# Optimization experiments

Measured on AMD Instinct MI355X. Metric: run time of the kernel, lower is better.

The kernel has to match this reference:

```python
import jax, jax.numpy as jnp
import numpy as np

B, S, D, H, HD, I = 8, 512, 2048, 32, 64, 8192
REL = 2 * 512 - 1  # 1023
EPS = 1e-6
SCALE = float(np.sqrt(HD))


def _layernorm(x, g, b):
    mu = jnp.mean(x, axis=-1, keepdims=True)
    var = jnp.mean(jnp.square(x - mu), axis=-1, keepdims=True)
    return (x - mu) / jnp.sqrt(var + EPS) * g + b


def setup_inputs() -> dict:
    key = jax.random.key(0)
    ks = jax.random.split(key, 10)
    s = 0.02
    return {
        "hidden_states": jax.random.normal(ks[0], (B, S, D), dtype=jnp.float32),
        "wq": jax.random.normal(ks[1], (D, D), dtype=jnp.float32) * s,
        "wk": jax.random.normal(ks[2], (D, D), dtype=jnp.float32) * s,
        "wv": jax.random.normal(ks[3], (D, D), dtype=jnp.float32) * s,
        "wo": jax.random.normal(ks[4], (D, D), dtype=jnp.float32) * s,
        "rel_pos": jax.random.normal(ks[5], (REL, HD), dtype=jnp.float32),
        "ln1_g": jnp.ones((D,), jnp.float32),
        "ln1_b": jnp.zeros((D,), jnp.float32),
        "gate_w": jax.random.normal(ks[6], (D, I), dtype=jnp.float32) * s,
        "up_w": jax.random.normal(ks[7], (D, I), dtype=jnp.float32) * s,
        "down_w": jax.random.normal(ks[8], (I, D), dtype=jnp.float32) * s,
        "ln2_g": jnp.ones((D,), jnp.float32),
        "ln2_b": jnp.zeros((D,), jnp.float32),
    }


def reference(hidden_states, wq, wk, wv, wo, rel_pos, ln1_g, ln1_b,
              gate_w, up_w, down_w, ln2_g, ln2_b):
    x = hidden_states
    # --- MultiHeadAttentionXL ---
    q = (x @ wq).reshape(B, S, H, HD)
    k = (x @ wk).reshape(B, S, H, HD)
    v = (x @ wv).reshape(B, S, H, HD)
    scores = jnp.einsum('bqhd,bkhd->bhqk', q, k) / SCALE
    # relative position bias (seq_len <= 512 path)
    pos = jnp.arange(S)
    rp = jnp.clip(pos[None, :] - pos[:, None] + 512 - 1, 0, REL - 1)  # [S,S]
    bias = rel_pos[rp].mean(axis=-1)  # [S,S]
    scores = scores + bias[None, None]
    attn = jax.nn.softmax(scores, axis=-1)
    ctx = jnp.einsum('bhqk,bkhd->bqhd', attn, v).reshape(B, S, D)
    attn_out = ctx @ wo
    # residual + post-LN
    h = _layernorm(x + attn_out, ln1_g, ln1_b)
    # --- FeedForwardXL (SwiGLU) ---
    gate = jax.nn.silu(h @ gate_w)
    up = h @ up_w
    ffn = (gate * up) @ down_w
    h = _layernorm(h + ffn, ln2_g, ln2_b)
    return h
```

## Files before the change

kernel.cpp:

```cpp
#include <hip/hip_runtime.h>
#include <cstdint>
#include <cstddef>

typedef _Float16 f16;
typedef _Float16 f16x8 __attribute__((ext_vector_type(8)));
typedef _Float16 f16x4 __attribute__((ext_vector_type(4)));
typedef float    f32x4 __attribute__((ext_vector_type(4)));

constexpr int S_ = 512, D_ = 2048, H_ = 32, HD_ = 64, I_ = 8192;
constexpr int M_ = 4096;
constexpr int IH_ = 4096;

enum { OP_F32 = 0, OP_QKT = 3, OP_PV = 4, OP_QKV = 6, OP_GU = 9, OP_ADD = 10 };

__device__ __forceinline__ void gl_lds16(const void* g, void* lds) {
  __builtin_amdgcn_global_load_lds(
      (const __attribute__((address_space(1))) void*)g,
      (__attribute__((address_space(3))) void*)lds, 16, 0, 0);
}

template <int BM, int BN, int WR, int WC, int OP, int BK>
__global__ __launch_bounds__(256, 2) void gemm_k(
    const f16* __restrict__ A, int lda,
    const f16* __restrict__ B, int ldb,
    void* __restrict__ Cp, int ldc,
    int K, int bh0, const float* __restrict__ relmean,
    const f16* __restrict__ B2) {
  static_assert(WR * WC == 4, "4-wave blocks assumed");
  static_assert(BK == 32 || BK == 64, "");
  constexpr bool GU = (OP == OP_GU);
  constexpr int WM = BM / WR, WN = BN / WC;
  constexpr int IM = WM / 16, IN = WN / 16;
  constexpr int RR = (BK == 64) ? 8 : 16;
  constexpr int CA = BM * BK / 2048;
  constexpr int CB = BN * BK / 2048;
  constexpr int KS = BK / 32;
  __shared__ __align__(16) f16 As[BM * BK];
  __shared__ __align__(16) f16 Bs[(GU ? 2 : 1) * BN * BK];
  const int tid = threadIdx.x, wave = tid >> 6, lane = tid & 63;
  const int wm = wave / WC, wn = wave % WC;
  const int bn = blockIdx.x, bm = blockIdx.y, bz = blockIdx.z;

  long aoff = 0, boff = 0;
  if constexpr (OP == OP_QKT) {
    int bh = bh0 + bz;
    long hb = (long)(bh >> 5) * (S_ * D_) + (long)(bh & (H_ - 1)) * HD_;
    aoff = hb; boff = hb;
  }
  if constexpr (OP == OP_PV) {
    int bh = bh0 + bz;
    aoff = (long)bz * S_ * S_;
    boff = (long)bh * HD_ * S_;
  }
  if constexpr (OP == OP_QKV) boff = (long)bz * D_ * D_;

  const f16* Ab = A + aoff + (long)bm * BM * lda;
  const f16* Bb = B + boff + (long)bn * BN * ldb;
  const f16* Bb2 = nullptr;
  if constexpr (GU) Bb2 = B2 + (long)bn * BN * ldb;

  f32x4 acc[IM][IN], acc2[GU ? IM : 1][GU ? IN : 1];
#pragma unroll
  for (int i = 0; i < IM; i++)
#pragma unroll
    for (int j = 0; j < IN; j++) {
      acc[i][j] = {0.f, 0.f, 0.f, 0.f};
      if constexpr (GU) acc2[i][j] = {0.f, 0.f, 0.f, 0.f};
    }

  const int lrr = (BK == 64) ? (lane >> 3) : (lane >> 2);
  const int lcc = (BK == 64) ? (lane & 7) : (lane & 3);
  const int scc = (BK == 64) ? (lcc ^ (lrr & 7)) : lcc;
  const int g = lane >> 4, l15 = lane & 15;

  for (int kt = 0; kt < K; kt += BK) {
    if (kt) __syncthreads();
#pragma unroll
    for (int c = 0; c < CA; c++) {
      int reg = wave * CA + c;
      gl_lds16(Ab + (long)(reg * RR + lrr) * lda + kt + scc * 8, &As[reg * 512]);
    }
#pragma unroll
    for (int c = 0; c < CB; c++) {
      int reg = wave * CB + c;
      gl_lds16(Bb + (long)(reg * RR + lrr) * ldb + kt + scc * 8, &Bs[reg * 512]);
      if constexpr (GU)
        gl_lds16(Bb2 + (long)(reg * RR + lrr) * ldb + kt + scc * 8,
                 &Bs[BN * BK + reg * 512]);
    }
    __syncthreads();
    f16x8 af[KS][IM], bf[KS][IN], bf2[GU ? KS : 1][GU ? IN : 1];
#pragma unroll
    for (int s = 0; s < KS; s++) {
#pragma unroll
      for (int i = 0; i < IM; i++) {
        int row = wm * WM + i * 16 + l15;
        int cidx = s * 4 + g;
        if constexpr (BK == 64) cidx ^= (row & 7);
        af[s][i] = *(const f16x8*)&As[row * BK + cidx * 8];
      }
#pragma unroll
      for (int j = 0; j < IN; j++) {
        int colL = wn * WN + j * 16 + l15;
        int cidx = s * 4 + g;
        if constexpr (BK == 64) cidx ^= (colL & 7);
        bf[s][j] = *(const f16x8*)&Bs[colL * BK + cidx * 8];
        if constexpr (GU) bf2[s][j] = *(const f16x8*)&Bs[BN * BK + colL * BK + cidx * 8];
      }
    }
#pragma unroll
    for (int s = 0; s < KS; s++)
#pragma unroll
      for (int i = 0; i < IM; i++)
#pragma unroll
        for (int j = 0; j < IN; j++) {
          acc[i][j] = __builtin_amdgcn_mfma_f32_16x16x32_f16(af[s][i], bf[s][j], acc[i][j], 0, 0, 0);
          if constexpr (GU)
            acc2[i][j] = __builtin_amdgcn_mfma_f32_16x16x32_f16(af[s][i], bf2[s][j], acc2[i][j], 0, 0, 0);
        }
  }

  const int r0 = bm * BM + wm * WM + (lane >> 4) * 4;
  const int c0 = bn * BN + wn * WN + l15;
#pragma unroll
  for (int i = 0; i < IM; i++) {
#pragma unroll
    for (int j = 0; j < IN; j++) {
      int rowb = r0 + i * 16;
      int col = c0 + j * 16;
      if constexpr (OP == OP_F32) {
        float* C = (float*)Cp;
#pragma unroll
        for (int t = 0; t < 4; t++) C[(long)(rowb + t) * ldc + col] = acc[i][j][t];
      } else if constexpr (OP == OP_ADD) {
        float* C = (float*)Cp;
#pragma unroll
        for (int t = 0; t < 4; t++) C[(long)(rowb + t) * ldc + col] += acc[i][j][t];
      } else if constexpr (OP == OP_GU) {
        f16* C = (f16*)Cp;
#pragma unroll
        for (int t = 0; t < 4; t++) {
          float gg = acc[i][j][t], u = acc2[i][j][t];
          C[(long)(rowb + t) * ldc + col] = (f16)(gg / (1.f + __expf(-gg)) * u);
        }
      } else if constexpr (OP == OP_QKT) {
        f16* C = (f16*)Cp + (long)bz * S_ * S_;
#pragma unroll
        for (int t = 0; t < 4; t++) {
          int r = rowb + t;
          C[(long)r * S_ + col] = (f16)(acc[i][j][t] * 0.125f + relmean[col - r + 511]);
        }
      } else if constexpr (OP == OP_PV) {
        int bh = bh0 + bz;
        f16* C = (f16*)Cp + (long)(bh >> 5) * (S_ * D_) + (long)(bh & (H_ - 1)) * HD_;
#pragma unroll
        for (int t = 0; t < 4; t++) C[(long)(rowb + t) * ldc + col] = (f16)acc[i][j][t];
      } else if constexpr (OP == OP_QKV) {
        f16* C = (f16*)Cp;
        if (bz < 2) {
          f16* Cq = C + (long)bz * M_ * D_;
#pragma unroll
          for (int t = 0; t < 4; t++) Cq[(long)(rowb + t) * ldc + col] = (f16)acc[i][j][t];
        } else {
          f16* Cv = C + (long)2 * M_ * D_;
          int b = rowb >> 9, s0 = rowb & 511, h = col >> 6, hd = col & 63;
          f16x4 pk;
#pragma unroll
          for (int t = 0; t < 4; t++) pk[t] = (f16)acc[i][j][t];
          *(f16x4*)&Cv[((long)(b * H_ + h) * HD_ + hd) * S_ + s0] = pk;
        }
      }
    }
  }
}

__global__ __launch_bounds__(512, 2) void fattn_k(
    const f16* __restrict__ Q, const f16* __restrict__ Kg,
    const f16* __restrict__ Vt, f16* __restrict__ Ctx,
    const float* __restrict__ rel) {
  __shared__ __align__(16) f16 Ks[512 * 64];
  __shared__ __align__(16) f16 Vs[64 * 512];
  __shared__ float rms[1024];
  const int tid = threadIdx.x, wave = tid >> 6, lane = tid & 63;
  const int g = lane >> 4, l15 = lane & 15;
  const int lrr = lane >> 3, lcc = lane & 7;
  const int bm = blockIdx.x, bh = blockIdx.y;
  const int b = bh >> 5, h = bh & 31;
  const long qrow0 = (long)b * S_ + bm * 128;
  const long krow0 = (long)b * S_;
  const int hoff = h * HD_;

#pragma unroll
  for (int c = 0; c < 8; c++) {
    int reg = wave * 8 + c;
    gl_lds16(Kg + (krow0 + reg * 8 + lrr) * D_ + hoff + (lcc ^ lrr) * 8,
             &Ks[reg * 512]);
  }
  const f16* vb = Vt + (long)bh * HD_ * S_;
#pragma unroll
  for (int c = 0; c < 8; c++) {
    int reg = wave * 8 + c;
    int rb = reg >> 3, cb = reg & 7;
    gl_lds16(vb + (long)(rb * 8 + lrr) * S_ + cb * 64 + (lcc ^ lrr) * 8,
             &Vs[reg * 512]);
  }
  for (int i = tid; i < 1023; i += 512) rms[i] = rel[i];

  f16x8 aq[2];
#pragma unroll
  for (int ks = 0; ks < 2; ks++)
    aq[ks] = *(const f16x8*)&Q[(qrow0 + wave * 16 + l15) * D_ + hoff + ks * 32 + g * 8];

  __syncthreads();

  f32x4 acc[32];
#pragma unroll
  for (int jn = 0; jn < 32; jn++) acc[jn] = {0.f, 0.f, 0.f, 0.f};
#pragma unroll
  for (int jn = 0; jn < 32; jn++) {
    int r = jn * 16 + l15;
    f16x8 b0 = *(const f16x8*)&Ks[r * 64 + ((g) ^ (r & 7)) * 8];
    f16x8 b1 = *(const f16x8*)&Ks[r * 64 + ((4 + g) ^ (r & 7)) * 8];
    acc[jn] = __builtin_amdgcn_mfma_f32_16x16x32_f16(aq[0], b0, acc[jn], 0, 0, 0);
    acc[jn] = __builtin_amdgcn_mfma_f32_16x16x32_f16(aq[1], b1, acc[jn], 0, 0, 0);
  }

  const int qr0 = bm * 128 + wave * 16 + g * 4;
  float mx[4] = {-1e30f, -1e30f, -1e30f, -1e30f}, sum[4] = {0.f, 0.f, 0.f, 0.f};
#pragma unroll
  for (int t = 0; t < 4; t++) {
    int bb = l15 - (qr0 + t) + 511;
#pragma unroll
    for (int jn = 0; jn < 32; jn++) {
      float v = acc[jn][t] * 0.125f + rms[bb + jn * 16];
      acc[jn][t] = v;
      mx[t] = fmaxf(mx[t], v);
    }
  }
#pragma unroll
  for (int off = 8; off; off >>= 1)
#pragma unroll
    for (int t = 0; t < 4; t++) mx[t] = fmaxf(mx[t], __shfl_xor(mx[t], off));
#pragma unroll
  for (int t = 0; t < 4; t++)
#pragma unroll
    for (int jn = 0; jn < 32; jn++) {
      float e = __expf(acc[jn][t] - mx[t]);
      acc[jn][t] = e;
      sum[t] += e;
    }
#pragma unroll
  for (int off = 8; off; off >>= 1)
#pragma unroll
    for (int t = 0; t < 4; t++) sum[t] += __shfl_xor(sum[t], off);
  float rs[4];
#pragma unroll
  for (int t = 0; t < 4; t++) rs[t] = 1.f / sum[t];

  __syncthreads();

  f16* Pb = &Ks[wave * 4096];
  f32x4 aco[4];
#pragma unroll
  for (int jv = 0; jv < 4; jv++) aco[jv] = {0.f, 0.f, 0.f, 0.f};
#pragma unroll
  for (int hh = 0; hh < 2; hh++) {
#pragma unroll
    for (int jl = 0; jl < 16; jl++) {
      int jn = hh * 16 + jl;
      f16x4 w;
#pragma unroll
      for (int t = 0; t < 4; t++) w[t] = (f16)(acc[jn][t] * rs[t]);
      *(f16x4*)&Pb[(jl * 16 + l15) * 16 + g * 4] = w;
    }
#pragma unroll
    for (int kl = 0; kl < 8; kl++) {
      f16x8 ap;
#pragma unroll
      for (int i = 0; i < 8; i++)
        ap[i] = Pb[(kl * 32 + g * 8 + i) * 16 + l15];
#pragma unroll
      for (int jv = 0; jv < 4; jv++) {
        int r = jv * 16 + l15, c = (hh * 8 + kl) * 4 + g;
        f16x8 bv = *(const f16x8*)&Vs[(r >> 3) * 4096 + (c >> 3) * 512 +
                                      (r & 7) * 64 + ((c & 7) ^ (r & 7)) * 8];
        aco[jv] = __builtin_amdgcn_mfma_f32_16x16x32_f16(ap, bv, aco[jv], 0, 0, 0);
      }
    }
  }

#pragma unroll
  for (int jv = 0; jv < 4; jv++)
#pragma unroll
    for (int t = 0; t < 4; t++)
      Ctx[(qrow0 + wave * 16 + g * 4 + t) * D_ + hoff + jv * 16 + l15] =
          (f16)aco[jv][t];
}

__global__ __launch_bounds__(256) void transpose_k(
    const float* __restrict__ in, int ldin, int k0, int n0,
    f16* __restrict__ out, int ldout) {
  __shared__ f16 t[64][68];
  const int kb = blockIdx.x * 64, nb = blockIdx.y * 64;
  const int tid = threadIdx.x;
  {
    const int kr = tid >> 4, nc = (tid & 15) * 4;
    const float* src = in + (long)(k0 + kb) * ldin + (n0 + nb);
#pragma unroll
    for (int i = 0; i < 4; i++) {
      int k = kr + i * 16;
      f32x4 v = *(const f32x4*)&src[(long)k * ldin + nc];
#pragma unroll
      for (int j = 0; j < 4; j++) t[nc + j][k] = (f16)v[j];
    }
  }
  __syncthreads();
  {
    const int n = tid >> 2, kc = (tid & 3) * 16;
    f16* dst = out + (long)(nb + n) * ldout + (kb + kc);
#pragma unroll
    for (int j = 0; j < 4; j++)
      *(f16x4*)&dst[j * 4] = *(const f16x4*)&t[n][kc + j * 4];
  }
}

__global__ void cvt_f16_k(const float* __restrict__ in, f16* __restrict__ out, int n4) {
  int i = blockIdx.x * 256 + threadIdx.x;
  if (i >= n4) return;
  f32x4 v = ((const f32x4*)in)[i];
  f16x4 o;
#pragma unroll
  for (int t = 0; t < 4; t++) o[t] = (f16)v[t];
  ((f16x4*)out)[i] = o;
}

__global__ void relmean_k(const float* __restrict__ rel, float* __restrict__ rm) {
  int i = blockIdx.x * 256 + threadIdx.x;
  if (i >= 1023) return;
  float s = 0.f;
#pragma unroll 8
  for (int d = 0; d < 64; d++) s += rel[i * 64 + d];
  rm[i] = s * (1.f / 64.f);
}

__global__ __launch_bounds__(256) void ln1_k(const float* __restrict__ X,
                                             const float* __restrict__ Y,
                                             const float* __restrict__ g,
                                             const float* __restrict__ b,
                                             f16* __restrict__ outH) {
  int row = blockIdx.x;
  const float* x = X + (long)row * D_;
  const float* y = Y + (long)row * D_;
  int t = threadIdx.x;
  float v[8], sum = 0.f, sq = 0.f;
#pragma unroll
  for (int i = 0; i < 8; i++) {
    int idx = t + i * 256;
    float val = x[idx] + y[idx];
    v[i] = val; sum += val; sq += val * val;
  }
  for (int off = 32; off; off >>= 1) { sum += __shfl_down(sum, off); sq += __shfl_down(sq, off); }
  __shared__ float s1[4], s2[4];
  if ((t & 63) == 0) { s1[t >> 6] = sum; s2[t >> 6] = sq; }
  __syncthreads();
  sum = s1[0] + s1[1] + s1[2] + s1[3];
  sq = s2[0] + s2[1] + s2[2] + s2[3];
  float mu = sum * (1.f / D_);
  float rstd = rsqrtf(sq * (1.f / D_) - mu * mu + 1e-6f);
#pragma unroll
  for (int i = 0; i < 8; i++) {
    int idx = t + i * 256;
    outH[(long)row * D_ + idx] = (f16)((v[i] - mu) * rstd * g[idx] + b[idx]);
  }
}

__global__ __launch_bounds__(256) void ln2f_k(const float* __restrict__ X,
                                              const f16* __restrict__ Y,
                                              const float* __restrict__ g,
                                              const float* __restrict__ b,
                                              float* __restrict__ outF) {
  int row = blockIdx.x;
  const float* x = X + (long)row * D_;
  const f16* y = Y + (long)row * D_;
  int t = threadIdx.x;
  float v[8], sum = 0.f, sq = 0.f;
#pragma unroll
  for (int i = 0; i < 8; i++) {
    int idx = t + i * 256;
    float val = x[idx] + (float)y[idx];
    v[i] = val; sum += val; sq += val * val;
  }
  for (int off = 32; off; off >>= 1) { sum += __shfl_down(sum, off); sq += __shfl_down(sq, off); }
  __shared__ float s1[4], s2[4];
  if ((t & 63) == 0) { s1[t >> 6] = sum; s2[t >> 6] = sq; }
  __syncthreads();
  sum = s1[0] + s1[1] + s1[2] + s1[3];
  sq = s2[0] + s2[1] + s2[2] + s2[3];
  float mu = sum * (1.f / D_);
  float rstd = rsqrtf(sq * (1.f / D_) - mu * mu + 1e-6f);
#pragma unroll
  for (int i = 0; i < 8; i++) {
    int idx = t + i * 256;
    outF[(long)row * D_ + idx] = (v[i] - mu) * rstd * g[idx] + b[idx];
  }
}

extern "C" void kernel_launch(void* const* d_in, const int* in_sizes, int n_in,
                              void* d_out, int out_size, void* d_ws, size_t ws_size,
                              hipStream_t stream) {
  const float* x    = (const float*)d_in[0];
  const float* wq   = (const float*)d_in[1];
  const float* wk   = (const float*)d_in[2];
  const float* wv   = (const float*)d_in[3];
  const float* wo   = (const float*)d_in[4];
  const float* rel  = (const float*)d_in[5];
  const float* ln1g = (const float*)d_in[6];
  const float* ln1b = (const float*)d_in[7];
  const float* gw   = (const float*)d_in[8];
  const float* uw   = (const float*)d_in[9];
  const float* dw   = (const float*)d_in[10];
  const float* ln2g = (const float*)d_in[11];
  const float* ln2b = (const float*)d_in[12];
  float* out = (float*)d_out;

  constexpr size_t MD2 = (size_t)M_ * D_ * 2;
  if (ws_size < 8 * MD2 + 4096) return;
  char* w = (char*)d_ws;
  f16* qb   = (f16*)(w + 0 * MD2);
  f16* vT   = (f16*)(w + 2 * MD2);
  f16* xb   = (f16*)(w + 3 * MD2);
  f16* s45  = (f16*)(w + 4 * MD2);
  f16* h1h  = (f16*)(w + 6 * MD2);
  f16* s7   = (f16*)(w + 7 * MD2);
  float* relmean = (float*)(w + 8 * MD2);
  f16* ctxb = xb;
  float* attn_out = (float*)qb;
  f16* wqT  = s45;
  f16* woT  = s7;
  f16* gwTh = qb;
  f16* uwTh = (f16*)(w + 1 * MD2);
  f16* gch  = vT;
  f16* dwTh = s7;
  float* facc = (float*)s45;

  cvt_f16_k<<<M_ * D_ / 4 / 256, 256, 0, stream>>>(x, xb, M_ * D_ / 4);
  relmean_k<<<4, 256, 0, stream>>>(rel, relmean);
  transpose_k<<<dim3(32, 32), 256, 0, stream>>>(wq, D_, 0, 0, wqT, D_);
  transpose_k<<<dim3(32, 32), 256, 0, stream>>>(wk, D_, 0, 0, wqT + (size_t)D_ * D_, D_);
  transpose_k<<<dim3(32, 32), 256, 0, stream>>>(wv, D_, 0, 0, wqT + 2 * (size_t)D_ * D_, D_);
  transpose_k<<<dim3(32, 32), 256, 0, stream>>>(wo, D_, 0, 0, woT, D_);

  gemm_k<128, 128, 2, 2, OP_QKV, 32><<<dim3(16, 32, 3), 256, 0, stream>>>(
      xb, D_, wqT, D_, qb, D_, D_, 0, nullptr, nullptr);

  fattn_k<<<dim3(4, 256), 512, 0, stream>>>(
      qb, qb + (size_t)M_ * D_, vT, ctxb, relmean);

  gemm_k<128, 128, 2, 2, OP_F32, 32><<<dim3(16, 32, 1), 256, 0, stream>>>(
      ctxb, D_, woT, D_, attn_out, D_, D_, 0, nullptr, nullptr);
  ln1_k<<<M_, 256, 0, stream>>>(x, attn_out, ln1g, ln1b, h1h);

  for (int h = 0; h < 2; h++) {
    transpose_k<<<dim3(32, 64), 256, 0, stream>>>(gw, I_, 0, h * IH_, gwTh, D_);
    transpose_k<<<dim3(32, 64), 256, 0, stream>>>(uw, I_, 0, h * IH_, uwTh, D_);
    transpose_k<<<dim3(64, 32), 256, 0, stream>>>(dw, D_, h * IH_, 0, dwTh, IH_);
    gemm_k<128, 128, 2, 2, OP_GU, 32><<<dim3(IH_ / 128, 32, 1), 256, 0, stream>>>(
        h1h, D_, gwTh, D_, gch, IH_, D_, 0, nullptr, uwTh);
    if (h == 0)
      gemm_k<128, 128, 2, 2, OP_F32, 32><<<dim3(16, 32, 1), 256, 0, stream>>>(
          gch, IH_, dwTh, IH_, facc, D_, IH_, 0, nullptr, nullptr);
    else
      gemm_k<128, 128, 2, 2, OP_ADD, 32><<<dim3(16, 32, 1), 256, 0, stream>>>(
          gch, IH_, dwTh, IH_, facc, D_, IH_, 0, nullptr, nullptr);
  }
  ln2f_k<<<M_, 256, 0, stream>>>(facc, h1h, ln2g, ln2b, out);
}
```

Measured before the change: 1.086 ms.

## Add 256x256 8-wave pipelined GEMM for QKV and split gate/up projections

Introduces a new 512-thread GEMM kernel with 256x256 tiles, 64-wide K steps, swizzled LDS, direct global-to-LDS loads and a four-phase interleaved load/MFMA schedule with priority hints. It replaces the 128x128 GEMM for the fused QKV projection. The combined gate/up kernel is split into a SiLU pass followed by an up pass that multiplies the stored gate in place. Larger tiles are meant to cut global/LDS traffic per FLOP and hide load latency, at the cost of an extra read/write of the gate buffer and more register pressure.

```diff
diff --git a/kernel.cpp b/kernel.cpp
--- a/kernel.cpp
+++ b/kernel.cpp
@@ -11,12 +11,178 @@
 constexpr int M_ = 4096;
 constexpr int IH_ = 4096;
 
-enum { OP_F32 = 0, OP_QKT = 3, OP_PV = 4, OP_QKV = 6, OP_GU = 9, OP_ADD = 10 };
+enum { OP_F32 = 0, OP_QKT = 3, OP_PV = 4, OP_QKV = 6, OP_GU = 9, OP_ADD = 10,
+       OP_SILU = 11, OP_UPG = 12 };
 
 __device__ __forceinline__ void gl_lds16(const void* g, void* lds) {
   __builtin_amdgcn_global_load_lds(
       (const __attribute__((address_space(1))) void*)g,
       (__attribute__((address_space(3))) void*)lds, 16, 0, 0);
+}
+
+template <int MH, int NH>
+__device__ __forceinline__ void mfma_q(f32x4 (&acc)[8][4],
+                                       const f16x8 (&ra)[2][4],
+                                       const f16x8 (&rb)[2][2]) {
+#pragma unroll
+  for (int ks = 0; ks < 2; ks++)
+#pragma unroll
+    for (int i = 0; i < 4; i++)
+#pragma unroll
+      for (int j = 0; j < 2; j++)
+        acc[MH * 4 + i][NH * 2 + j] = __builtin_amdgcn_mfma_f32_16x16x32_f16(
+            ra[ks][i], rb[ks][j], acc[MH * 4 + i][NH * 2 + j], 0, 0, 0);
+}
+
+template <int OP>
+__global__ __launch_bounds__(512, 2) void gemm8_k(
+    const f16* __restrict__ A, int lda,
+    const f16* __restrict__ B, int ldb,
+    void* __restrict__ Cp, int ldc, int K,
+    const f16* __restrict__ G) {
+  __shared__ __align__(16) f16 As[2 * 2 * 128 * 64];
+  __shared__ __align__(16) f16 Bs[2 * 2 * 128 * 64];
+  const int tid = threadIdx.x, wave = tid >> 6, lane = tid & 63;
+  const int wm = wave >> 2, wn = wave & 3;
+  const int g = lane >> 4, l15 = lane & 15;
+  const int lr8 = lane >> 3, lc8 = lane & 7;
+  const int bn = blockIdx.x, bm = blockIdx.y;
+  const f16* Ab = A + (long)bm * 256 * lda;
+  const f16* Bb = B + (long)bn * 256 * ldb;
+  const int sc_src = lc8 ^ (((lr8 >> 2) & 1) << 1);
+  const int swz_rd = ((l15 >> 2) & 1) << 1;
+
+  f32x4 acc[8][4];
+#pragma unroll
+  for (int i = 0; i < 8; i++)
+#pragma unroll
+    for (int j = 0; j < 4; j++) acc[i][j] = {0.f, 0.f, 0.f, 0.f};
+
+  int aoff[2][4], boff[2][2];
+#pragma unroll
+  for (int ks = 0; ks < 2; ks++) {
+#pragma unroll
+    for (int i = 0; i < 4; i++)
+      aoff[ks][i] = (i * 16 + l15) * 64 + ((ks * 4 + g) ^ swz_rd) * 8;
+#pragma unroll
+    for (int j = 0; j < 2; j++)
+      boff[ks][j] = ((wn & 1) * 64 + j * 16 + l15) * 64 + ((ks * 4 + g) ^ swz_rd) * 8;
+  }
+
+  auto stA = [&](int buf, int half, int kt) {
+#pragma unroll
+    for (int c = 0; c < 2; c++)
+      gl_lds16(Ab + (long)(half * 128 + (wave * 2 + c) * 8 + lr8) * lda + kt + sc_src * 8,
+               &As[buf * 16384 + half * 8192 + (wave * 2 + c) * 512]);
+  };
+  auto stB = [&](int buf, int half, int kt) {
+#pragma unroll
+    for (int c = 0; c < 2; c++)
+      gl_lds16(Bb + (long)(half * 128 + (wave * 2 + c) * 8 + lr8) * ldb + kt + sc_src * 8,
+               &Bs[buf * 16384 + half * 8192 + (wave * 2 + c) * 512]);
+  };
+
+  const int NT = K / 64;
+  stB(0, 0, 0); stB(0, 1, 0); stA(0, 0, 0); stA(0, 1, 0);
+  stB(1, 0, 64); stB(1, 1, 64);
+  asm volatile("s_waitcnt vmcnt(4)" ::: "memory");
+  __builtin_amdgcn_s_barrier();
+
+  f16x8 ra[2][4], rb0[2][2], rb1[2][2];
+  for (int T = 0; T < NT; T++) {
+    const int buf = T & 1, kt = T * 64;
+    const f16* Ah = &As[buf * 16384 + wm * 8192];
+    const f16* Bh = &Bs[buf * 16384 + (wn >> 1) * 8192];
+#pragma unroll
+    for (int ks = 0; ks < 2; ks++) {
+#pragma unroll
+      for (int i = 0; i < 4; i++) ra[ks][i] = *(const f16x8*)&Ah[aoff[ks][i]];
+#pragma unroll
+      for (int j = 0; j < 2; j++) rb0[ks][j] = *(const f16x8*)&Bh[boff[ks][j]];
+    }
+    if (T + 1 < NT) stA(buf ^ 1, 0, kt + 64);
+    __builtin_amdgcn_s_barrier();
+    asm volatile("s_waitcnt lgkmcnt(0)" ::: "memory");
+    __builtin_amdgcn_sched_barrier(0);
+    __builtin_amdgcn_s_setprio(1);
+    mfma_q<0, 0>(acc, ra, rb0);
+    __builtin_amdgcn_s_setprio(0);
+    __builtin_amdgcn_s_barrier();
+#pragma unroll
+    for (int ks = 0; ks < 2; ks++)
+#pragma unroll
+      for (int j = 0; j < 2; j++) rb1[ks][j] = *(const f16x8*)&Bh[2048 + boff[ks][j]];
+    if (T + 1 < NT) stA(buf ^ 1, 1, kt + 64);
+    __builtin_amdgcn_s_barrier();
+    asm volatile("s_waitcnt lgkmcnt(0)" ::: "memory");
+    __builtin_amdgcn_sched_barrier(0);
+    __builtin_amdgcn_s_setprio(1);
+    mfma_q<0, 1>(acc, ra, rb1);
+    __builtin_amdgcn_s_setprio(0);
+    __builtin_amdgcn_s_barrier();
+#pragma unroll
+    for (int ks = 0; ks < 2; ks++)
+#pragma unroll
+      for (int i = 0; i < 4; i++) ra[ks][i] = *(const f16x8*)&Ah[4096 + aoff[ks][i]];
+    if (T + 2 < NT) stB(buf, 0, kt + 128);
+    __builtin_amdgcn_s_barrier();
+    asm volatile("s_waitcnt lgkmcnt(0)" ::: "memory");
+    __builtin_amdgcn_sched_barrier(0);
+    __builtin_amdgcn_s_setprio(1);
+    mfma_q<1, 1>(acc, ra, rb1);
+    __builtin_amdgcn_s_setprio(0);
+    __builtin_amdgcn_s_barrier();
+    if (T + 2 < NT) stB(buf, 1, kt + 128);
+    __builtin_amdgcn_s_barrier();
+    __builtin_amdgcn_s_setprio(1);
+    mfma_q<1, 0>(acc, ra, rb0);
+    __builtin_amdgcn_s_setprio(0);
+    if (T < NT - 2) asm volatile("s_waitcnt vmcnt(4)" ::: "memory");
+    else            asm volatile("s_waitcnt vmcnt(0)" ::: "memory");
+    __builtin_amdgcn_s_barrier();
+  }
+
+  const int r0 = bm * 256 + wm * 128 + g * 4;
+  const int c0 = bn * 256 + wn * 64 + l15;
+#pragma unroll
+  for (int mi = 0; mi < 8; mi++) {
+#pragma unroll
+    for (int nj = 0; nj < 4; nj++) {
+      int rowb = r0 + mi * 16;
+      int col = c0 + nj * 16;
+      if constexpr (OP == OP_SILU) {
+        f16* C = (f16*)Cp;
+#pragma unroll
+        for (int t = 0; t < 4; t++) {
+          float v = acc[mi][nj][t];
+          C[(long)(rowb + t) * ldc + col] = (f16)(v / (1.f + __expf(-v)));
+        }
+      } else if constexpr (OP == OP_UPG) {
+        f16* C = (f16*)Cp;
+#pragma unroll
+        for (int t = 0; t < 4; t++) {
+          long idx = (long)(rowb + t) * ldc + col;
+          C[idx] = (f16)((float)G[idx] * acc[mi][nj][t]);
+        }
+      } else if constexpr (OP == OP_QKV) {
+        f16* C = (f16*)Cp;
+        if (bn < 16) {
+          f16* Cq = C + (bn >= 8 ? (long)M_ * D_ : 0);
+          int cc = col & 2047;
+#pragma unroll
+          for (int t = 0; t < 4; t++) Cq[(long)(rowb + t) * D_ + cc] = (f16)acc[mi][nj][t];
+        } else {
+          f16* Cv = C + (long)2 * M_ * D_;
+          int colv = col - 4096;
+          int b = rowb >> 9, s0 = rowb & 511, h = colv >> 6, hd = colv & 63;
+          f16x4 pk;
+#pragma unroll
+          for (int t = 0; t < 4; t++) pk[t] = (f16)acc[mi][nj][t];
+          *(f16x4*)&Cv[((long)(b * H_ + h) * HD_ + hd) * S_ + s0] = pk;
+        }
+      }
+    }
+  }
 }
 
 template <int BM, int BN, int WR, int WC, int OP, int BK>
@@ -450,8 +616,8 @@
   transpose_k<<<dim3(32, 32), 256, 0, stream>>>(wv, D_, 0, 0, wqT + 2 * (size_t)D_ * D_, D_);
   transpose_k<<<dim3(32, 32), 256, 0, stream>>>(wo, D_, 0, 0, woT, D_);
 
-  gemm_k<128, 128, 2, 2, OP_QKV, 32><<<dim3(16, 32, 3), 256, 0, stream>>>(
-      xb, D_, wqT, D_, qb, D_, D_, 0, nullptr, nullptr);
+  gemm8_k<OP_QKV><<<dim3(24, 16), 512, 0, stream>>>(
+      xb, D_, wqT, D_, qb, D_, D_, nullptr);
 
   fattn_k<<<dim3(4, 256), 512, 0, stream>>>(
       qb, qb + (size_t)M_ * D_, vT, ctxb, relmean);
@@ -464,8 +630,10 @@
     transpose_k<<<dim3(32, 64), 256, 0, stream>>>(gw, I_, 0, h * IH_, gwTh, D_);
     transpose_k<<<dim3(32, 64), 256, 0, stream>>>(uw, I_, 0, h * IH_, uwTh, D_);
     transpose_k<<<dim3(64, 32), 256, 0, stream>>>(dw, D_, h * IH_, 0, dwTh, IH_);
-    gemm_k<128, 128, 2, 2, OP_GU, 32><<<dim3(IH_ / 128, 32, 1), 256, 0, stream>>>(
-        h1h, D_, gwTh, D_, gch, IH_, D_, 0, nullptr, uwTh);
+    gemm8_k<OP_SILU><<<dim3(16, 16), 512, 0, stream>>>(
+        h1h, D_, gwTh, D_, gch, IH_, D_, nullptr);
+    gemm8_k<OP_UPG><<<dim3(16, 16), 512, 0, stream>>>(
+        h1h, D_, uwTh, D_, gch, IH_, D_, gch);
     if (h == 0)
       gemm_k<128, 128, 2, 2, OP_F32, 32><<<dim3(16, 32, 1), 256, 0, stream>>>(
           gch, IH_, dwTh, IH_, facc, D_, IH_, 0, nullptr, nullptr);
```

Result: faster. 1.054 ms (-2.9%).
